# Optimization experiments

Hardware: AMD Instinct MI355X
Metric: run time of the kernel (lower is better)

Reference implementation:

```python
import jax, jax.numpy as jnp
import numpy as np

D_MODEL = 1024
N_HEADS = 16
D_K = D_MODEL // N_HEADS
SEQ = 2048
BATCH = 2
THETA = 10000.0


def _rope(x, token_positions):
    # x: [b, h, s, dk]; token_positions: [s] int
    k = jnp.arange(0, D_K, 2, dtype=jnp.float32)
    freqs = 1.0 / (THETA ** (k / D_K))                    # [dk/2]
    angles = token_positions.astype(jnp.float32)[:, None] * freqs[None, :]  # [s, dk/2]
    cos = jnp.cos(angles)
    sin = jnp.sin(angles)
    x1 = x[..., 0::2]
    x2 = x[..., 1::2]
    r1 = x1 * cos - x2 * sin
    r2 = x1 * sin + x2 * cos
    out = jnp.stack([r1, r2], axis=-1)                    # [b,h,s,dk/2,2]
    return out.reshape(x.shape)


def setup_inputs() -> dict:
    key = jax.random.key(0)
    ks = jax.random.split(key, 5)
    sigma = np.sqrt(2.0 / (D_MODEL + D_MODEL))
    x = jax.random.normal(ks[0], (BATCH, SEQ, D_MODEL), dtype=jnp.float32)
    Wq = jax.random.truncated_normal(ks[1], -3.0, 3.0, (D_MODEL, D_MODEL), dtype=jnp.float32) * sigma
    Wk = jax.random.truncated_normal(ks[2], -3.0, 3.0, (D_MODEL, D_MODEL), dtype=jnp.float32) * sigma
    Wv = jax.random.truncated_normal(ks[3], -3.0, 3.0, (D_MODEL, D_MODEL), dtype=jnp.float32) * sigma
    Wo = jax.random.truncated_normal(ks[4], -3.0, 3.0, (D_MODEL, D_MODEL), dtype=jnp.float32) * sigma
    token_positions = jnp.arange(SEQ, dtype=jnp.int64)
    return {"x": x, "Wq": Wq, "Wk": Wk, "Wv": Wv, "Wo": Wo, "token_positions": token_positions}


def reference(x, Wq, Wk, Wv, Wo, token_positions):
    b, s, d = x.shape
    # projections: Linear stores weight [out,in], applies x @ W.T
    Q = x @ Wq.T
    K = x @ Wk.T
    V = x @ Wv.T
    # [b, s, h*dk] -> [b, h, s, dk]
    def split_heads(t):
        return t.reshape(b, s, N_HEADS, D_K).transpose(0, 2, 1, 3)
    Q, K, V = split_heads(Q), split_heads(K), split_heads(V)
    Q = _rope(Q, token_positions)
    K = _rope(K, token_positions)
    scale = 1.0 / np.sqrt(D_K).astype(np.float32)
    scores = jnp.einsum('bhqd,bhkd->bhqk', Q, K) * scale   # [b,h,s,s]
    causal = jnp.tril(jnp.ones((s, s), dtype=bool))
    scores = jnp.where(causal, scores, -jnp.inf)
    attn = jax.nn.softmax(scores, axis=-1)
    out = jnp.einsum('bhqk,bhkd->bhqd', attn, V)           # [b,h,s,dk]
    out = out.transpose(0, 2, 1, 3).reshape(b, s, d)
    return out @ Wo.T
```

## Files before the change

kernel.cpp:

```cpp
#include <hip/hip_runtime.h>
#include <hip/hip_bf16.h>
#include <stdint.h>

#define SEQL   2048
#define NBATCH 2
#define BSZ    4096
#define DMODEL 1024
#define NH     16
#define DK     64
#define NBH    32
#define NCHUNK_TOT 40

typedef __attribute__((ext_vector_type(8)))  short short8;
typedef __attribute__((ext_vector_type(4)))  short shortx4;
typedef __attribute__((ext_vector_type(4)))  float f32x4;
typedef __attribute__((ext_vector_type(16))) float f32x16;
typedef __attribute__((ext_vector_type(4)))  unsigned uint4v;
union PU { uint4v u; short8 s; };

__device__ __forceinline__ short f2b(float f) {
  unsigned u = __float_as_uint(f);
  u = (u + 0x7FFF + ((u >> 16) & 1)) >> 16;
  return (short)u;
}
__device__ __forceinline__ float b2f(short s) {
  return __uint_as_float(((unsigned)(unsigned short)s) << 16);
}
__device__ __forceinline__ unsigned cvtpk(float lo, float hi) {
  unsigned r;
  asm("v_cvt_pk_bf16_f32 %0, %1, %2" : "=v"(r) : "v"(lo), "v"(hi));
  return r;
}
#define PLSWAP(a_, b_) asm("v_permlane32_swap_b32 %0, %1" : "+v"(a_), "+v"(b_))

__device__ __forceinline__ void g2l16(const void* g, void* l) {
  __builtin_amdgcn_global_load_lds(
      (__attribute__((address_space(1))) void*)(uintptr_t)g,
      (__attribute__((address_space(3))) void*)l, 16, 0, 0);
}

__device__ __forceinline__ f32x4 mfma16(short8 a, short8 b, f32x4 c) {
  return __builtin_amdgcn_mfma_f32_16x16x32_bf16(a, b, c, 0, 0, 0);
}
__device__ __forceinline__ f32x16 mfma32(short8 a, short8 b, f32x16 c) {
  return __builtin_amdgcn_mfma_f32_32x32x16_bf16(a, b, c, 0, 0, 0);
}

__global__ void cvt_all(const float* __restrict__ x,  const float* __restrict__ wq,
                        const float* __restrict__ wk, const float* __restrict__ wv,
                        const float* __restrict__ wo, short* __restrict__ xb,
                        short* __restrict__ wqkv, short* __restrict__ wob) {
  long idx = ((long)blockIdx.x * 256 + threadIdx.x) * 4;
  const float* s; short* d; long off;
  if (idx < 4194304L)      { s = x;  d = xb;             off = idx; }
  else if (idx < 5242880L) { s = wq; d = wqkv;           off = idx - 4194304L; }
  else if (idx < 6291456L) { s = wk; d = wqkv + 1048576; off = idx - 5242880L; }
  else if (idx < 7340032L) { s = wv; d = wqkv + 2097152; off = idx - 6291456L; }
  else                     { s = wo; d = wob;            off = idx - 7340032L; }
  float4 v = *(const float4*)(s + off);
  shortx4 r;
  r[0] = f2b(v.x); r[1] = f2b(v.y); r[2] = f2b(v.z); r[3] = f2b(v.w);
  *(shortx4*)(d + off) = r;
}

__global__ __launch_bounds__(512, 1)
void gemm256(const short* __restrict__ A, const short* __restrict__ B,
             const int* __restrict__ tok, short* __restrict__ qh,
             short* __restrict__ kh, short* __restrict__ vlin) {
  __shared__ short As[2][16384];
  __shared__ short Bs[2][12288];
  int id = blockIdx.x;
  int swz = (id & 7) * 32 + (id >> 3);
  int bm = swz >> 4, bn = swz & 15;
  int brow = bm << 8, bcoln = bn * 192;
  int tid = threadIdx.x, w = tid >> 6;
  int wm = w >> 2, wn = w & 3;
  int lr = tid & 15, lg = (tid >> 4) & 3;
  const short* Abase = A + (long)brow * 1024;
  const short* Bbase = B + (long)bcoln * 1024;

  f32x4 acc[8][3];
#pragma unroll
  for (int mi = 0; mi < 8; ++mi)
#pragma unroll
    for (int ni = 0; ni < 3; ++ni) acc[mi][ni] = (f32x4){0.f, 0.f, 0.f, 0.f};

#define STGA(s_, kt_, buf_) do {                                                \
    int r_ = tid >> 3, gch_ = (tid & 7) ^ (r_ & 7);                             \
    g2l16(Abase + (long)((s_) * 64 + r_) * 1024 + (kt_) * 64 + gch_ * 8,        \
          &As[buf_][(s_) * 4096 + tid * 8]); } while (0)
#define STGB(s_, kt_, buf_) do {                                                \
    int r_ = tid >> 3, gch_ = (tid & 7) ^ (r_ & 7);                             \
    g2l16(Bbase + (long)((s_) * 64 + r_) * 1024 + (kt_) * 64 + gch_ * 8,        \
          &Bs[buf_][(s_) * 4096 + tid * 8]); } while (0)

  STGA(0,0,0); STGA(1,0,0); STGA(2,0,0); STGA(3,0,0);
  STGB(0,0,0); STGB(1,0,0); STGB(2,0,0);
  STGA(0,1,1); STGA(1,1,1); STGA(2,1,1); STGA(3,1,1);
  STGB(0,1,1); STGB(1,1,1); STGB(2,1,1);
  asm volatile("s_waitcnt vmcnt(7)" ::: "memory");
  __builtin_amdgcn_s_barrier();

  for (int kt = 0; kt < 16; ++kt) {
    int cur = kt & 1;
    const short* Ah = &As[cur][wm * 8192];
    const short* Bh = &Bs[cur][0];
    short8 a0[4][2], a1[4][2], bf[3][2];
#pragma unroll
    for (int mi = 0; mi < 4; ++mi) {
      int rin = mi * 16 + lr;
#pragma unroll
      for (int ks = 0; ks < 2; ++ks)
        a0[mi][ks] = *(const short8*)
            &Ah[rin * 64 + (((ks * 4 + lg) ^ (rin & 7)) << 3)];
    }
#pragma unroll
    for (int ni = 0; ni < 3; ++ni) {
      int ci = wn * 48 + ni * 16 + lr;
      int sub = ci >> 6, rin = ci & 63;
#pragma unroll
      for (int ks = 0; ks < 2; ++ks)
        bf[ni][ks] = *(const short8*)
            &Bh[sub * 4096 + rin * 64 + (((ks * 4 + lg) ^ (rin & 7)) << 3)];
    }
#pragma unroll
    for (int mi = 0; mi < 4; ++mi) {
      int rin = mi * 16 + lr;
#pragma unroll
      for (int ks = 0; ks < 2; ++ks)
        a1[mi][ks] = *(const short8*)
            &Ah[4096 + rin * 64 + (((ks * 4 + lg) ^ (rin & 7)) << 3)];
    }
    __builtin_amdgcn_s_setprio(1);
#pragma unroll
    for (int mi = 0; mi < 4; ++mi)
#pragma unroll
      for (int ni = 0; ni < 3; ++ni)
#pragma unroll
        for (int ks = 0; ks < 2; ++ks)
          acc[mi][ni] = mfma16(a0[mi][ks], bf[ni][ks], acc[mi][ni]);
    __builtin_amdgcn_s_setprio(0);
    asm volatile("s_waitcnt lgkmcnt(0)" ::: "memory");
    __builtin_amdgcn_s_barrier();
    if (kt + 2 < 16) {
      STGA(0, kt + 2, cur); STGA(1, kt + 2, cur);
      STGA(2, kt + 2, cur); STGA(3, kt + 2, cur);
      STGB(0, kt + 2, cur); STGB(1, kt + 2, cur); STGB(2, kt + 2, cur);
    }
    __builtin_amdgcn_s_setprio(1);
#pragma unroll
    for (int mi = 0; mi < 4; ++mi)
#pragma unroll
      for (int ni = 0; ni < 3; ++ni)
#pragma unroll
        for (int ks = 0; ks < 2; ++ks)
          acc[mi + 4][ni] = mfma16(a1[mi][ks], bf[ni][ks], acc[mi + 4][ni]);
    __builtin_amdgcn_s_setprio(0);
    if (kt + 1 < 16) {
      if (kt + 2 < 16) asm volatile("s_waitcnt vmcnt(7)" ::: "memory");
      else             asm volatile("s_waitcnt vmcnt(0)" ::: "memory");
    }
    __builtin_amdgcn_s_barrier();
  }
#undef STGA
#undef STGB

  int sbase = brow + wm * 128;
#pragma unroll
  for (int ni = 0; ni < 3; ++ni) {
    int gcol = bcoln + wn * 48 + ni * 16 + lr;
    int mat = gcol >> 10;
    int cin = gcol & 1023;
    if (mat == 2) {
#pragma unroll
      for (int mi = 0; mi < 8; ++mi)
#pragma unroll
        for (int rr = 0; rr < 4; ++rr) {
          int grow = sbase + mi * 16 + lg * 4 + rr;
          vlin[(long)grow * 1024 + cin] = f2b(acc[mi][ni][rr]);
        }
    } else {
      short* dst = mat ? kh : qh;
      float scale = mat ? 1.0f : 0.125f * 1.44269504f;
      int d = cin & 63, h = cin >> 6;
      int i = d >> 1;
      int odd = d & 1;
      float frev = exp2f(-(float)i * 0.41524101186f) * 0.15915494309f;
#pragma unroll
      for (int mi = 0; mi < 8; ++mi)
#pragma unroll
        for (int rr = 0; rr < 4; ++rr) {
          int grow = sbase + mi * 16 + lg * 4 + rr;
          int s = grow & 2047, b = grow >> 11;
          float pos = (float)tok[s];
          float rev = pos * frev;
          float fr = rev - floorf(rev);
          float sn, cs;
          asm("v_sin_f32 %0, %1" : "=v"(sn) : "v"(fr));
          asm("v_cos_f32 %0, %1" : "=v"(cs) : "v"(fr));
          float v = acc[mi][ni][rr];
          float p = __shfl_xor(v, 1);
          float out = odd ? (p * sn + v * cs) : (v * cs - p * sn);
          dst[((long)(b * 16 + h) * 2048 + s) * 64 + d] = f2b(out * scale);
        }
    }
  }
}

__global__ __launch_bounds__(256, 2)
void gemm_fin(const short* __restrict__ A, const short* __restrict__ B,
              float* __restrict__ C) {
  __shared__ short As[2][8192];
  __shared__ short Bs[2][8192];
  int bm = blockIdx.x >> 3, bn = blockIdx.x & 7;
  int tid = threadIdx.x, w = tid >> 6, l = tid & 63;
  int wm = w >> 1, wn = w & 1;
  int lr = l & 15, lg = l >> 4;
  int brow = bm << 7, bcol = bn << 7;
  const short* Abase = A + (long)brow * 1024;
  const short* Bbase = B + (long)bcol * 1024;

  const f32x4 fz = {0.f, 0.f, 0.f, 0.f};
  f32x4 acc[4][4];
#pragma unroll
  for (int xi = 0; xi < 4; ++xi)
#pragma unroll
    for (int yi = 0; yi < 4; ++yi) acc[xi][yi] = fz;

#define FSTG(kt_, buf_) do {                                                    \
    _Pragma("unroll")                                                           \
    for (int i_ = 0; i_ < 4; ++i_) {                                            \
      int idx_ = i_ * 256 + tid;                                                \
      int r_ = idx_ >> 3, gch_ = (idx_ & 7) ^ (r_ & 7);                         \
      g2l16(Abase + (long)r_ * 1024 + (kt_) * 64 + gch_ * 8,                    \
            &As[buf_][idx_ * 8]);                                               \
      g2l16(Bbase + (long)r_ * 1024 + (kt_) * 64 + gch_ * 8,                    \
            &Bs[buf_][idx_ * 8]);                                               \
    } } while (0)

  FSTG(0, 0);
  FSTG(1, 1);
  asm volatile("s_waitcnt vmcnt(8)" ::: "memory");
  __builtin_amdgcn_s_barrier();

  for (int kt = 0; kt < 16; ++kt) {
    int cur = kt & 1;
    short8 af[4][2], bfr[4][2];
#pragma unroll
    for (int xi = 0; xi < 4; ++xi) {
      int ar = wm * 64 + xi * 16 + lr;
      int br = wn * 64 + xi * 16 + lr;
#pragma unroll
      for (int ks = 0; ks < 2; ++ks) {
        af[xi][ks] = *(const short8*)
            &As[cur][ar * 64 + (((ks * 4 + lg) ^ (ar & 7)) << 3)];
        bfr[xi][ks] = *(const short8*)
            &Bs[cur][br * 64 + (((ks * 4 + lg) ^ (br & 7)) << 3)];
      }
    }
    __builtin_amdgcn_s_setprio(1);
#pragma unroll
    for (int xi = 0; xi < 4; ++xi)
#pragma unroll
      for (int yi = 0; yi < 4; ++yi)
        acc[xi][yi] = mfma16(af[xi][0], bfr[yi][0], acc[xi][yi]);
    __builtin_amdgcn_s_setprio(0);
    asm volatile("s_waitcnt lgkmcnt(0)" ::: "memory");
    __builtin_amdgcn_s_barrier();
    if (kt + 2 < 16) FSTG(kt + 2, cur);
    __builtin_amdgcn_s_setprio(1);
#pragma unroll
    for (int xi = 0; xi < 4; ++xi)
#pragma unroll
      for (int yi = 0; yi < 4; ++yi)
        acc[xi][yi] = mfma16(af[xi][1], bfr[yi][1], acc[xi][yi]);
    __builtin_amdgcn_s_setprio(0);
    if (kt + 1 < 16) {
      if (kt + 2 < 16) asm volatile("s_waitcnt vmcnt(8)" ::: "memory");
      else             asm volatile("s_waitcnt vmcnt(0)" ::: "memory");
    }
    __builtin_amdgcn_s_barrier();
  }
#undef FSTG

#pragma unroll
  for (int xi = 0; xi < 4; ++xi)
#pragma unroll
    for (int yi = 0; yi < 4; ++yi)
#pragma unroll
      for (int r = 0; r < 4; ++r) {
        int row = brow + wm * 64 + xi * 16 + lg * 4 + r;
        int col = bcol + wn * 64 + yi * 16 + lr;
        C[(long)row * 1024 + col] = acc[xi][yi][r];
      }
}

__global__ void vtrans(const short* __restrict__ Vlin, short* __restrict__ Vt) {
  __shared__ short tile[64][72];
  int s0 = blockIdx.x * 64;
  int bh = blockIdx.y;
  int b = bh >> 4, h = bh & 15;
  int t = threadIdx.x;
  int r = t >> 2, c0 = (t & 3) * 16;
  const short* src = Vlin + ((long)(b * 2048 + s0 + r)) * 1024 + h * 64 + c0;
  *(short8*)&tile[r][c0]     = *(const short8*)src;
  *(short8*)&tile[r][c0 + 8] = *(const short8*)(src + 8);
  __syncthreads();
  int d = t >> 2, sc0 = (t & 3) * 16;
  short8 o0, o1;
#pragma unroll
  for (int j = 0; j < 8; ++j) { o0[j] = tile[sc0 + j][d]; o1[j] = tile[sc0 + 8 + j][d]; }
  short* dst = Vt + ((long)(bh * 64 + d)) * 2048 + s0 + sc0;
  *(short8*)dst       = o0;
  *(short8*)(dst + 8) = o1;
}

__global__ __launch_bounds__(256, 3)
void attn_fwd(const short* __restrict__ Qh, const short* __restrict__ Kh,
              const short* __restrict__ Vt, short* __restrict__ poO,
              float* __restrict__ pmb, float* __restrict__ plb) {
  __shared__ short Ks[3][4096];
  __shared__ short Vs[3][4096];
  int bh = blockIdx.x;
  int xr = 39 - blockIdx.y;
  int qi, c = xr, nc = 1;
  for (qi = 0; qi < 16; ++qi) { nc = (qi >> 2) + 1; if (c < nc) break; c -= nc; }
  int n = 2 * qi + 2;
  int t0 = (c * n) / nc, t1 = ((c + 1) * n) / nc;
  int q0b = qi << 7;
  int tid = threadIdx.x, w = tid >> 6, l = tid & 63;
  int ql = l & 31, hi = l >> 5;
  const short* Qb = Qh + (long)bh * (2048 * 64);
  const short* Kb = Kh + (long)bh * (2048 * 64);
  const short* Vb = Vt + (long)bh * (64 * 2048);
  int qw = q0b + 32 * w;
  int qg = qw + ql;
  int pid = bh * NCHUNK_TOT + xr;

  short8 qf[4];
#pragma unroll
  for (int kc = 0; kc < 4; ++kc)
    qf[kc] = *(const short8*)(Qb + (long)qg * 64 + kc * 16 + hi * 8);

  f32x16 o0, o1;
#pragma unroll
  for (int r = 0; r < 16; ++r) { o0[r] = 0.f; o1[r] = 0.f; }
  float m = -1e30f, lsum = 0.f;

#define STAGE(t_, bufi_) do {                                                   \
    int s0_ = (t_) << 6;                                                        \
    _Pragma("unroll")                                                           \
    for (int i_ = 0; i_ < 2; ++i_) {                                            \
      int c_ = w + 4 * i_;                                                      \
      int g_ = c_ >> 2, cc_ = c_ & 3;                                           \
      g2l16(Kb + ((long)(s0_ + g_ * 32 + ql)) * 64 + cc_ * 16 + hi * 8,         \
            &Ks[bufi_][c_ * 512]);                                              \
      g2l16(Vb + ((long)(g_ * 32 + ql)) * 2048 + s0_ + cc_ * 16 + hi * 8,       \
            &Vs[bufi_][c_ * 512]);                                              \
    }                                                                           \
  } while (0)

  STAGE(t0, 0);
  if (t0 + 1 < t1) STAGE(t0 + 1, 1);
  int cur = 0;

  for (int t = t0; t < t1; ++t) {
    if (t + 2 < t1) {
      int nb = cur + 2; if (nb >= 3) nb -= 3;
      STAGE(t + 2, nb);
      asm volatile("s_waitcnt vmcnt(8)" ::: "memory");
    } else if (t + 1 < t1) {
      asm volatile("s_waitcnt vmcnt(4)" ::: "memory");
    } else {
      asm volatile("s_waitcnt vmcnt(0)" ::: "memory");
    }
    __builtin_amdgcn_s_barrier();
    int s0 = t << 6;
    if (s0 <= qw + 31) {
      bool upper = (s0 + 32 <= qw + 31);
      f32x16 sT0, sT1;
#pragma unroll
      for (int r = 0; r < 16; ++r) { sT0[r] = 0.f; sT1[r] = 0.f; }
      __builtin_amdgcn_s_setprio(1);
#pragma unroll
      for (int kc = 0; kc < 4; ++kc) {
        short8 k0 = *(const short8*)&Ks[cur][(kc * 64 + l) * 8];
        sT0 = mfma32(k0, qf[kc], sT0);
      }
      if (upper) {
#pragma unroll
        for (int kc = 0; kc < 4; ++kc) {
          short8 k1 = *(const short8*)&Ks[cur][((4 + kc) * 64 + l) * 8];
          sT1 = mfma32(k1, qf[kc], sT1);
        }
      }
      __builtin_amdgcn_s_setprio(0);
      if (s0 + 63 > qw) {
#pragma unroll
        for (int r = 0; r < 16; ++r) {
          int kvl = (r & 3) + 8 * (r >> 2) + 4 * hi;
          if (s0 + kvl > qg) sT0[r] = -1e30f;
        }
        if (upper) {
#pragma unroll
          for (int r = 0; r < 16; ++r) {
            int kvl = (r & 3) + 8 * (r >> 2) + 4 * hi;
            if (s0 + 32 + kvl > qg) sT1[r] = -1e30f;
          }
        }
      }
      float pmax = sT0[0];
#pragma unroll
      for (int r = 1; r < 16; ++r) pmax = fmaxf(pmax, sT0[r]);
      if (upper) {
#pragma unroll
        for (int r = 0; r < 16; ++r) pmax = fmaxf(pmax, sT1[r]);
      }
      pmax = fmaxf(pmax, __shfl_xor(pmax, 32));
      if (__any(pmax > m + 11.5416f)) {
        float mn = fmaxf(m, pmax);
        float sf = exp2f(m - mn);
        m = mn;
        lsum *= sf;
#pragma unroll
        for (int r = 0; r < 16; ++r) {
          int row = (r & 3) + 8 * (r >> 2) + 4 * hi;
          float fo = __shfl(sf, row);
          o0[r] *= fo; o1[r] *= fo;
        }
      }
      float rs = 0.f;
#pragma unroll
      for (int r = 0; r < 16; ++r) {
        float p = exp2f(sT0[r] - m);
        sT0[r] = p; rs += p;
      }
      if (upper) {
#pragma unroll
        for (int r = 0; r < 16; ++r) {
          float p = exp2f(sT1[r] - m);
          sT1[r] = p; rs += p;
        }
      }
      rs += __shfl_xor(rs, 32);
      lsum += rs;
      short8 pa[4];
      {
        unsigned cA[4], cB[4];
#pragma unroll
        for (int g = 0; g < 4; ++g) {
          cA[g] = cvtpk(sT0[4 * g], sT0[4 * g + 1]);
          cB[g] = cvtpk(sT0[4 * g + 2], sT0[4 * g + 3]);
        }
        PLSWAP(cA[0], cA[1]); PLSWAP(cB[0], cB[1]);
        PLSWAP(cA[2], cA[3]); PLSWAP(cB[2], cB[3]);
        PU p0; p0.u = (uint4v){cA[0], cB[0], cA[1], cB[1]}; pa[0] = p0.s;
        PU p1; p1.u = (uint4v){cA[2], cB[2], cA[3], cB[3]}; pa[1] = p1.s;
      }
      if (upper) {
        unsigned cA[4], cB[4];
#pragma unroll
        for (int g = 0; g < 4; ++g) {
          cA[g] = cvtpk(sT1[4 * g], sT1[4 * g + 1]);
          cB[g] = cvtpk(sT1[4 * g + 2], sT1[4 * g + 3]);
        }
        PLSWAP(cA[0], cA[1]); PLSWAP(cB[0], cB[1]);
        PLSWAP(cA[2], cA[3]); PLSWAP(cB[2], cB[3]);
        PU p2; p2.u = (uint4v){cA[0], cB[0], cA[1], cB[1]}; pa[2] = p2.s;
        PU p3; p3.u = (uint4v){cA[2], cB[2], cA[3], cB[3]}; pa[3] = p3.s;
      }
      __builtin_amdgcn_s_setprio(1);
#pragma unroll
      for (int kc = 0; kc < 2; ++kc) {
        short8 v0 = *(const short8*)&Vs[cur][(kc * 64 + l) * 8];
        short8 v1 = *(const short8*)&Vs[cur][((4 + kc) * 64 + l) * 8];
        o0 = mfma32(pa[kc], v0, o0);
        o1 = mfma32(pa[kc], v1, o1);
      }
      if (upper) {
#pragma unroll
        for (int kc = 2; kc < 4; ++kc) {
          short8 v0 = *(const short8*)&Vs[cur][(kc * 64 + l) * 8];
          short8 v1 = *(const short8*)&Vs[cur][((4 + kc) * 64 + l) * 8];
          o0 = mfma32(pa[kc], v0, o0);
          o1 = mfma32(pa[kc], v1, o1);
        }
      }
      __builtin_amdgcn_s_setprio(0);
    }
    asm volatile("s_waitcnt lgkmcnt(0)" ::: "memory");
    __builtin_amdgcn_s_barrier();
    ++cur; if (cur >= 3) cur -= 3;
  }
#undef STAGE

  if (hi == 0) {
    pmb[pid * 128 + w * 32 + ql] = m;
    plb[pid * 128 + w * 32 + ql] = lsum;
  }
#pragma unroll
  for (int r = 0; r < 16; ++r) {
    int row = (r & 3) + 8 * (r >> 2) + 4 * hi;
    long basep = ((long)pid * 128 + w * 32 + row) * 64;
    poO[basep + ql]      = f2b(o0[r]);
    poO[basep + 32 + ql] = f2b(o1[r]);
  }
}

__global__ void attn_combine(const short* __restrict__ poO,
                             const float* __restrict__ pmb,
                             const float* __restrict__ plb,
                             short* __restrict__ Oh) {
  int x = blockIdx.x, bh = blockIdx.y;
  int qi = x >> 2, sub = x & 3;
  int t = threadIdx.x;
  int r = sub * 32 + (t >> 3);
  int d0 = (t & 7) * 8;
  int nc = (qi >> 2) + 1;
  int prefix = 0;
  for (int j = 0; j < qi; ++j) prefix += (j >> 2) + 1;
  int base = bh * NCHUNK_TOT + prefix;
  float M = -1e30f;
  for (int i = 0; i < nc; ++i)
    M = fmaxf(M, pmb[(base + i) * 128 + r]);
  float acc0 = 0, acc1 = 0, acc2 = 0, acc3 = 0, acc4 = 0, acc5 = 0, acc6 = 0, acc7 = 0;
  float den = 0.f;
  for (int i = 0; i < nc; ++i) {
    float wgt = exp2f(pmb[(base + i) * 128 + r] - M);
    den += wgt * plb[(base + i) * 128 + r];
    short8 ov = *(const short8*)&poO[((long)(base + i) * 128 + r) * 64 + d0];
    acc0 += wgt * b2f(ov[0]); acc1 += wgt * b2f(ov[1]);
    acc2 += wgt * b2f(ov[2]); acc3 += wgt * b2f(ov[3]);
    acc4 += wgt * b2f(ov[4]); acc5 += wgt * b2f(ov[5]);
    acc6 += wgt * b2f(ov[6]); acc7 += wgt * b2f(ov[7]);
  }
  float inv = 1.0f / den;
  int b = bh >> 4, h = bh & 15;
  int s = qi * 128 + r;
  short8 out;
  out[0] = f2b(acc0 * inv); out[1] = f2b(acc1 * inv);
  out[2] = f2b(acc2 * inv); out[3] = f2b(acc3 * inv);
  out[4] = f2b(acc4 * inv); out[5] = f2b(acc5 * inv);
  out[6] = f2b(acc6 * inv); out[7] = f2b(acc7 * inv);
  *(short8*)&Oh[((long)(b * 2048 + s)) * 1024 + h * 64 + d0] = out;
}

extern "C" void kernel_launch(void* const* d_in, const int* in_sizes, int n_in,
                              void* d_out, int out_size, void* d_ws, size_t ws_size,
                              hipStream_t stream) {
  const float* x  = (const float*)d_in[0];
  const float* wq = (const float*)d_in[1];
  const float* wk = (const float*)d_in[2];
  const float* wv = (const float*)d_in[3];
  const float* wo = (const float*)d_in[4];
  const int* tok  = (const int*)d_in[5];

  short* wsp  = (short*)d_ws;
  short* xb   = wsp;
  short* wqkv = xb + 4194304;
  short* wob  = wqkv + 3145728;
  short* qkv  = wob + 1048576;
  short* qh   = qkv + 12582912;
  short* kh   = qh + 4194304;
  short* vt   = kh + 4194304;
  short* oh   = vt + 4194304;

  short* vlin = qkv + 8388608;
  short* poO = qkv;
  float* pmb = (float*)xb;
  float* plb = pmb + NCHUNK_TOT * NBH * 128;

  (void)in_sizes; (void)n_in; (void)out_size; (void)ws_size;

  cvt_all<<<8192, 256, 0, stream>>>(x, wq, wk, wv, wo, xb, wqkv, wob);
  gemm256<<<256, 512, 0, stream>>>(xb, wqkv, tok, qh, kh, vlin);
  vtrans<<<dim3(32, 32), 256, 0, stream>>>(vlin, vt);
  attn_fwd<<<dim3(32, NCHUNK_TOT), 256, 0, stream>>>(qh, kh, vt, poO, pmb, plb);
  attn_combine<<<dim3(64, 32), 256, 0, stream>>>(poO, pmb, plb, oh);
  gemm_fin<<<256, 256, 0, stream>>>(oh, wob, (float*)d_out);
}
```

Before: 118.5 us.

## Process two 128-row query groups per attention block to reuse staged K/V tiles

Each attention block now covers 256 query rows: every wave keeps two query fragments, two sets of softmax state and two pairs of accumulators, and runs the score/softmax/PV body twice on each staged K/V tile. This halves the number of KV-split work items (40 to 20 chunks per head) and the global-to-LDS traffic per query row, and the combine kernel is updated to match. In exchange the grid shrinks to 640 blocks, register pressure roughly doubles for accumulators, which risks spills or lower occupancy, and causal imbalance between the two halves leaves some work idle.

```diff
diff --git a/kernel.cpp b/kernel.cpp
--- a/kernel.cpp
+++ b/kernel.cpp
@@ -9,7 +9,7 @@
 #define NH     16
 #define DK     64
 #define NBH    32
-#define NCHUNK_TOT 40
+#define NCHUNK2 20
 
 typedef __attribute__((ext_vector_type(8)))  short short8;
 typedef __attribute__((ext_vector_type(4)))  short shortx4;
@@ -322,30 +322,33 @@
   __shared__ short Ks[3][4096];
   __shared__ short Vs[3][4096];
   int bh = blockIdx.x;
-  int xr = 39 - blockIdx.y;
+  int xr = NCHUNK2 - 1 - blockIdx.y;
   int qi, c = xr, nc = 1;
-  for (qi = 0; qi < 16; ++qi) { nc = (qi >> 2) + 1; if (c < nc) break; c -= nc; }
-  int n = 2 * qi + 2;
+  for (qi = 0; qi < 8; ++qi) { nc = (qi + 2) >> 1; if (c < nc) break; c -= nc; }
+  int n = 4 * qi + 4;
   int t0 = (c * n) / nc, t1 = ((c + 1) * n) / nc;
-  int q0b = qi << 7;
+  int q0b = qi << 8;
   int tid = threadIdx.x, w = tid >> 6, l = tid & 63;
   int ql = l & 31, hi = l >> 5;
   const short* Qb = Qh + (long)bh * (2048 * 64);
   const short* Kb = Kh + (long)bh * (2048 * 64);
   const short* Vb = Vt + (long)bh * (64 * 2048);
-  int qw = q0b + 32 * w;
-  int qg = qw + ql;
-  int pid = bh * NCHUNK_TOT + xr;
-
-  short8 qf[4];
-#pragma unroll
-  for (int kc = 0; kc < 4; ++kc)
-    qf[kc] = *(const short8*)(Qb + (long)qg * 64 + kc * 16 + hi * 8);
-
-  f32x16 o0, o1;
-#pragma unroll
-  for (int r = 0; r < 16; ++r) { o0[r] = 0.f; o1[r] = 0.f; }
-  float m = -1e30f, lsum = 0.f;
+  int qw0 = q0b + 32 * w;
+  int qw1 = q0b + 128 + 32 * w;
+  int qg0 = qw0 + ql, qg1 = qw1 + ql;
+  int pid = bh * NCHUNK2 + xr;
+
+  short8 qf0[4], qf1[4];
+#pragma unroll
+  for (int kc = 0; kc < 4; ++kc) {
+    qf0[kc] = *(const short8*)(Qb + (long)qg0 * 64 + kc * 16 + hi * 8);
+    qf1[kc] = *(const short8*)(Qb + (long)qg1 * 64 + kc * 16 + hi * 8);
+  }
+
+  f32x16 oA0, oB0, oA1, oB1;
+#pragma unroll
+  for (int r = 0; r < 16; ++r) { oA0[r] = 0.f; oB0[r] = 0.f; oA1[r] = 0.f; oB1[r] = 0.f; }
+  float m0 = -1e30f, l0 = 0.f, m1 = -1e30f, l1 = 0.f;
 
 #define STAGE(t_, bufi_) do {                                                   \
     int s0_ = (t_) << 6;                                                        \
@@ -360,6 +363,121 @@
     }                                                                           \
   } while (0)
 
+#define GBODY(qw_, qg_, qf_, m_, lsum_, oA_, oB_) do {                          \
+    if (s0 <= (qw_) + 31) {                                                     \
+      bool upper = (s0 + 32 <= (qw_) + 31);                                     \
+      f32x16 sT0, sT1;                                                          \
+      _Pragma("unroll")                                                         \
+      for (int r = 0; r < 16; ++r) { sT0[r] = 0.f; sT1[r] = 0.f; }              \
+      __builtin_amdgcn_s_setprio(1);                                            \
+      _Pragma("unroll")                                                         \
+      for (int kc = 0; kc < 4; ++kc) {                                          \
+        short8 k0 = *(const short8*)&Ks[cur][(kc * 64 + l) * 8];                \
+        sT0 = mfma32(k0, qf_[kc], sT0);                                         \
+      }                                                                         \
+      if (upper) {                                                              \
+        _Pragma("unroll")                                                       \
+        for (int kc = 0; kc < 4; ++kc) {                                        \
+          short8 k1 = *(const short8*)&Ks[cur][((4 + kc) * 64 + l) * 8];        \
+          sT1 = mfma32(k1, qf_[kc], sT1);                                       \
+        }                                                                       \
+      }                                                                         \
+      __builtin_amdgcn_s_setprio(0);                                            \
+      if (s0 + 63 > (qw_)) {                                                    \
+        _Pragma("unroll")                                                       \
+        for (int r = 0; r < 16; ++r) {                                          \
+          int kvl = (r & 3) + 8 * (r >> 2) + 4 * hi;                            \
+          if (s0 + kvl > (qg_)) sT0[r] = -1e30f;                                \
+        }                                                                       \
+        if (upper) {                                                            \
+          _Pragma("unroll")                                                     \
+          for (int r = 0; r < 16; ++r) {                                        \
+            int kvl = (r & 3) + 8 * (r >> 2) + 4 * hi;                          \
+            if (s0 + 32 + kvl > (qg_)) sT1[r] = -1e30f;                         \
+          }                                                                     \
+        }                                                                       \
+      }                                                                         \
+      float pmax = sT0[0];                                                      \
+      _Pragma("unroll")                                                         \
+      for (int r = 1; r < 16; ++r) pmax = fmaxf(pmax, sT0[r]);                  \
+      if (upper) {                                                              \
+        _Pragma("unroll")                                                       \
+        for (int r = 0; r < 16; ++r) pmax = fmaxf(pmax, sT1[r]);                \
+      }                                                                         \
+      pmax = fmaxf(pmax, __shfl_xor(pmax, 32));                                 \
+      if (__any(pmax > (m_) + 11.5416f)) {                                      \
+        float mn = fmaxf((m_), pmax);                                           \
+        float sf = exp2f((m_) - mn);                                            \
+        (m_) = mn;                                                              \
+        (lsum_) *= sf;                                                          \
+        _Pragma("unroll")                                                       \
+        for (int r = 0; r < 16; ++r) {                                          \
+          int row = (r & 3) + 8 * (r >> 2) + 4 * hi;                            \
+          float fo = __shfl(sf, row);                                           \
+          oA_[r] *= fo; oB_[r] *= fo;                                           \
+        }                                                                       \
+      }                                                                         \
+      float rs = 0.f;                                                           \
+      _Pragma("unroll")                                                         \
+      for (int r = 0; r < 16; ++r) {                                            \
+        float p = exp2f(sT0[r] - (m_));                                         \
+        sT0[r] = p; rs += p;                                                    \
+      }                                                                         \
+      if (upper) {                                                              \
+        _Pragma("unroll")                                                       \
+        for (int r = 0; r < 16; ++r) {                                          \
+          float p = exp2f(sT1[r] - (m_));                                       \
+          sT1[r] = p; rs += p;                                                  \
+        }                                                                       \
+      }                                                                         \
+      rs += __shfl_xor(rs, 32);                                                 \
+      (lsum_) += rs;                                                            \
+      short8 pa[4];                                                             \
+      {                                                                         \
+        unsigned cA[4], cB[4];                                                  \
+        _Pragma("unroll")                                                       \
+        for (int g = 0; g < 4; ++g) {                                           \
+          cA[g] = cvtpk(sT0[4 * g], sT0[4 * g + 1]);                            \
+          cB[g] = cvtpk(sT0[4 * g + 2], sT0[4 * g + 3]);                        \
+        }                                                                       \
+        PLSWAP(cA[0], cA[1]); PLSWAP(cB[0], cB[1]);                             \
+        PLSWAP(cA[2], cA[3]); PLSWAP(cB[2], cB[3]);                             \
+        PU p0; p0.u = (uint4v){cA[0], cB[0], cA[1], cB[1]}; pa[0] = p0.s;       \
+        PU p1; p1.u = (uint4v){cA[2], cB[2], cA[3], cB[3]}; pa[1] = p1.s;       \
+      }                                                                         \
+      if (upper) {                                                              \
+        unsigned cA[4], cB[4];                                                  \
+        _Pragma("unroll")                                                       \
+        for (int g = 0; g < 4; ++g) {                                           \
+          cA[g] = cvtpk(sT1[4 * g], sT1[4 * g + 1]);                            \
+          cB[g] = cvtpk(sT1[4 * g + 2], sT1[4 * g + 3]);                        \
+        }                                                                       \
+        PLSWAP(cA[0], cA[1]); PLSWAP(cB[0], cB[1]);                             \
+        PLSWAP(cA[2], cA[3]); PLSWAP(cB[2], cB[3]);                             \
+        PU p2; p2.u = (uint4v){cA[0], cB[0], cA[1], cB[1]}; pa[2] = p2.s;       \
+        PU p3; p3.u = (uint4v){cA[2], cB[2], cA[3], cB[3]}; pa[3] = p3.s;       \
+      }                                                                         \
+      __builtin_amdgcn_s_setprio(1);                                            \
+      _Pragma("unroll")                                                         \
+      for (int kc = 0; kc < 2; ++kc) {                                          \
+        short8 v0 = *(const short8*)&Vs[cur][(kc * 64 + l) * 8];                \
+        short8 v1 = *(const short8*)&Vs[cur][((4 + kc) * 64 + l) * 8];          \
+        oA_ = mfma32(pa[kc], v0, oA_);                                          \
+        oB_ = mfma32(pa[kc], v1, oB_);                                          \
+      }                                                                         \
+      if (upper) {                                                              \
+        _Pragma("unroll")                                                       \
+        for (int kc = 2; kc < 4; ++kc) {                                        \
+          short8 v0 = *(const short8*)&Vs[cur][(kc * 64 + l) * 8];              \
+          short8 v1 = *(const short8*)&Vs[cur][((4 + kc) * 64 + l) * 8];        \
+          oA_ = mfma32(pa[kc], v0, oA_);                                        \
+          oB_ = mfma32(pa[kc], v1, oB_);                                        \
+        }                                                                       \
+      }                                                                         \
+      __builtin_amdgcn_s_setprio(0);                                            \
+    }                                                                           \
+  } while (0)
+
   STAGE(t0, 0);
   if (t0 + 1 < t1) STAGE(t0 + 1, 1);
   int cur = 0;
@@ -376,134 +494,30 @@
     }
     __builtin_amdgcn_s_barrier();
     int s0 = t << 6;
-    if (s0 <= qw + 31) {
-      bool upper = (s0 + 32 <= qw + 31);
-      f32x16 sT0, sT1;
-#pragma unroll
-      for (int r = 0; r < 16; ++r) { sT0[r] = 0.f; sT1[r] = 0.f; }
-      __builtin_amdgcn_s_setprio(1);
-#pragma unroll
-      for (int kc = 0; kc < 4; ++kc) {
-        short8 k0 = *(const short8*)&Ks[cur][(kc * 64 + l) * 8];
-        sT0 = mfma32(k0, qf[kc], sT0);
-      }
-      if (upper) {
-#pragma unroll
-        for (int kc = 0; kc < 4; ++kc) {
-          short8 k1 = *(const short8*)&Ks[cur][((4 + kc) * 64 + l) * 8];
-          sT1 = mfma32(k1, qf[kc], sT1);
-        }
-      }
-      __builtin_amdgcn_s_setprio(0);
-      if (s0 + 63 > qw) {
-#pragma unroll
-        for (int r = 0; r < 16; ++r) {
-          int kvl = (r & 3) + 8 * (r >> 2) + 4 * hi;
-          if (s0 + kvl > qg) sT0[r] = -1e30f;
-        }
-        if (upper) {
-#pragma unroll
-          for (int r = 0; r < 16; ++r) {
-            int kvl = (r & 3) + 8 * (r >> 2) + 4 * hi;
-            if (s0 + 32 + kvl > qg) sT1[r] = -1e30f;
-          }
-        }
-      }
-      float pmax = sT0[0];
-#pragma unroll
-      for (int r = 1; r < 16; ++r) pmax = fmaxf(pmax, sT0[r]);
-      if (upper) {
-#pragma unroll
-        for (int r = 0; r < 16; ++r) pmax = fmaxf(pmax, sT1[r]);
-      }
-      pmax = fmaxf(pmax, __shfl_xor(pmax, 32));
-      if (__any(pmax > m + 11.5416f)) {
-        float mn = fmaxf(m, pmax);
-        float sf = exp2f(m - mn);
-        m = mn;
-        lsum *= sf;
-#pragma unroll
-        for (int r = 0; r < 16; ++r) {
-          int row = (r & 3) + 8 * (r >> 2) + 4 * hi;
-          float fo = __shfl(sf, row);
-          o0[r] *= fo; o1[r] *= fo;
-        }
-      }
-      float rs = 0.f;
-#pragma unroll
-      for (int r = 0; r < 16; ++r) {
-        float p = exp2f(sT0[r] - m);
-        sT0[r] = p; rs += p;
-      }
-      if (upper) {
-#pragma unroll
-        for (int r = 0; r < 16; ++r) {
-          float p = exp2f(sT1[r] - m);
-          sT1[r] = p; rs += p;
-        }
-      }
-      rs += __shfl_xor(rs, 32);
-      lsum += rs;
-      short8 pa[4];
-      {
-        unsigned cA[4], cB[4];
-#pragma unroll
-        for (int g = 0; g < 4; ++g) {
-          cA[g] = cvtpk(sT0[4 * g], sT0[4 * g + 1]);
-          cB[g] = cvtpk(sT0[4 * g + 2], sT0[4 * g + 3]);
-        }
-        PLSWAP(cA[0], cA[1]); PLSWAP(cB[0], cB[1]);
-        PLSWAP(cA[2], cA[3]); PLSWAP(cB[2], cB[3]);
-        PU p0; p0.u = (uint4v){cA[0], cB[0], cA[1], cB[1]}; pa[0] = p0.s;
-        PU p1; p1.u = (uint4v){cA[2], cB[2], cA[3], cB[3]}; pa[1] = p1.s;
-      }
-      if (upper) {
-        unsigned cA[4], cB[4];
-#pragma unroll
-        for (int g = 0; g < 4; ++g) {
-          cA[g] = cvtpk(sT1[4 * g], sT1[4 * g + 1]);
-          cB[g] = cvtpk(sT1[4 * g + 2], sT1[4 * g + 3]);
-        }
-        PLSWAP(cA[0], cA[1]); PLSWAP(cB[0], cB[1]);
-        PLSWAP(cA[2], cA[3]); PLSWAP(cB[2], cB[3]);
-        PU p2; p2.u = (uint4v){cA[0], cB[0], cA[1], cB[1]}; pa[2] = p2.s;
-        PU p3; p3.u = (uint4v){cA[2], cB[2], cA[3], cB[3]}; pa[3] = p3.s;
-      }
-      __builtin_amdgcn_s_setprio(1);
-#pragma unroll
-      for (int kc = 0; kc < 2; ++kc) {
-        short8 v0 = *(const short8*)&Vs[cur][(kc * 64 + l) * 8];
-        short8 v1 = *(const short8*)&Vs[cur][((4 + kc) * 64 + l) * 8];
-        o0 = mfma32(pa[kc], v0, o0);
-        o1 = mfma32(pa[kc], v1, o1);
-      }
-      if (upper) {
-#pragma unroll
-        for (int kc = 2; kc < 4; ++kc) {
-          short8 v0 = *(const short8*)&Vs[cur][(kc * 64 + l) * 8];
-          short8 v1 = *(const short8*)&Vs[cur][((4 + kc) * 64 + l) * 8];
-          o0 = mfma32(pa[kc], v0, o0);
-          o1 = mfma32(pa[kc], v1, o1);
-        }
-      }
-      __builtin_amdgcn_s_setprio(0);
-    }
+    GBODY(qw0, qg0, qf0, m0, l0, oA0, oB0);
+    GBODY(qw1, qg1, qf1, m1, l1, oA1, oB1);
     asm volatile("s_waitcnt lgkmcnt(0)" ::: "memory");
     __builtin_amdgcn_s_barrier();
     ++cur; if (cur >= 3) cur -= 3;
   }
 #undef STAGE
+#undef GBODY
 
   if (hi == 0) {
-    pmb[pid * 128 + w * 32 + ql] = m;
-    plb[pid * 128 + w * 32 + ql] = lsum;
+    pmb[pid * 256 + w * 32 + ql]       = m0;
+    plb[pid * 256 + w * 32 + ql]       = l0;
+    pmb[pid * 256 + 128 + w * 32 + ql] = m1;
+    plb[pid * 256 + 128 + w * 32 + ql] = l1;
   }
 #pragma unroll
   for (int r = 0; r < 16; ++r) {
     int row = (r & 3) + 8 * (r >> 2) + 4 * hi;
-    long basep = ((long)pid * 128 + w * 32 + row) * 64;
-    poO[basep + ql]      = f2b(o0[r]);
-    poO[basep + 32 + ql] = f2b(o1[r]);
+    long base0 = ((long)pid * 256 + w * 32 + row) * 64;
+    long base1 = ((long)pid * 256 + 128 + w * 32 + row) * 64;
+    poO[base0 + ql]      = f2b(oA0[r]);
+    poO[base0 + 32 + ql] = f2b(oB0[r]);
+    poO[base1 + ql]      = f2b(oA1[r]);
+    poO[base1 + 32 + ql] = f2b(oB1[r]);
   }
 }
 
@@ -512,23 +526,23 @@
                              const float* __restrict__ plb,
                              short* __restrict__ Oh) {
   int x = blockIdx.x, bh = blockIdx.y;
-  int qi = x >> 2, sub = x & 3;
+  int qi = x >> 3, sub = x & 7;
   int t = threadIdx.x;
   int r = sub * 32 + (t >> 3);
   int d0 = (t & 7) * 8;
-  int nc = (qi >> 2) + 1;
+  int nc = (qi + 2) >> 1;
   int prefix = 0;
-  for (int j = 0; j < qi; ++j) prefix += (j >> 2) + 1;
-  int base = bh * NCHUNK_TOT + prefix;
+  for (int j = 0; j < qi; ++j) prefix += (j + 2) >> 1;
+  int base = bh * NCHUNK2 + prefix;
   float M = -1e30f;
   for (int i = 0; i < nc; ++i)
-    M = fmaxf(M, pmb[(base + i) * 128 + r]);
+    M = fmaxf(M, pmb[(base + i) * 256 + r]);
   float acc0 = 0, acc1 = 0, acc2 = 0, acc3 = 0, acc4 = 0, acc5 = 0, acc6 = 0, acc7 = 0;
   float den = 0.f;
   for (int i = 0; i < nc; ++i) {
-    float wgt = exp2f(pmb[(base + i) * 128 + r] - M);
-    den += wgt * plb[(base + i) * 128 + r];
-    short8 ov = *(const short8*)&poO[((long)(base + i) * 128 + r) * 64 + d0];
+    float wgt = exp2f(pmb[(base + i) * 256 + r] - M);
+    den += wgt * plb[(base + i) * 256 + r];
+    short8 ov = *(const short8*)&poO[((long)(base + i) * 256 + r) * 64 + d0];
     acc0 += wgt * b2f(ov[0]); acc1 += wgt * b2f(ov[1]);
     acc2 += wgt * b2f(ov[2]); acc3 += wgt * b2f(ov[3]);
     acc4 += wgt * b2f(ov[4]); acc5 += wgt * b2f(ov[5]);
@@ -536,7 +550,7 @@
   }
   float inv = 1.0f / den;
   int b = bh >> 4, h = bh & 15;
-  int s = qi * 128 + r;
+  int s = qi * 256 + r;
   short8 out;
   out[0] = f2b(acc0 * inv); out[1] = f2b(acc1 * inv);
   out[2] = f2b(acc2 * inv); out[3] = f2b(acc3 * inv);
@@ -568,14 +582,14 @@
   short* vlin = qkv + 8388608;
   short* poO = qkv;
   float* pmb = (float*)xb;
-  float* plb = pmb + NCHUNK_TOT * NBH * 128;
+  float* plb = pmb + NCHUNK2 * NBH * 256;
 
   (void)in_sizes; (void)n_in; (void)out_size; (void)ws_size;
 
   cvt_all<<<8192, 256, 0, stream>>>(x, wq, wk, wv, wo, xb, wqkv, wob);
   gemm256<<<256, 512, 0, stream>>>(xb, wqkv, tok, qh, kh, vlin);
   vtrans<<<dim3(32, 32), 256, 0, stream>>>(vlin, vt);
-  attn_fwd<<<dim3(32, NCHUNK_TOT), 256, 0, stream>>>(qh, kh, vt, poO, pmb, plb);
+  attn_fwd<<<dim3(32, NCHUNK2), 256, 0, stream>>>(qh, kh, vt, poO, pmb, plb);
   attn_combine<<<dim3(64, 32), 256, 0, stream>>>(poO, pmb, plb, oh);
   gemm_fin<<<256, 256, 0, stream>>>(oh, wob, (float*)d_out);
 }
```

Result: slower. 137.0 us (+15.6%).
